# Kernel optimization log

Measured on AMD Instinct MI355X. Metric: run time of the kernel, lower is better.

Reference implementation:

```python
import jax, jax.numpy as jnp
import numpy as np

N1 = 1_000_000
N2 = 1_000_000
C = 64
M = 1_500_000


def setup_inputs() -> dict:
    key = jax.random.key(0)
    k1, k2, k3, k4, k5, k6 = jax.random.split(key, 6)
    feat1 = jax.random.normal(k1, (N1, C), dtype=jnp.float32)
    feat2 = jax.random.normal(k2, (N2, C), dtype=jnp.float32)
    # union_map[0] gathers each input row exactly once -> permutation
    map1_in = jax.random.permutation(k3, N1).astype(jnp.int32)
    map2_in = jax.random.permutation(k4, N2).astype(jnp.int32)
    # union_map[1]: output row each input point lands in
    map1_out = jax.random.randint(k5, (N1,), 0, M, dtype=jnp.int32)
    map2_out = jax.random.randint(k6, (N2,), 0, M, dtype=jnp.int32)
    return {
        "feat1": feat1, "feat2": feat2,
        "map1_in": map1_in, "map1_out": map1_out,
        "map2_in": map2_in, "map2_out": map2_out,
        "out_size": M,
    }


def reference(feat1, feat2, map1_in, map1_out, map2_in, map2_out, out_size):
    # out_feat[union_map[1]] += in_feat[union_map[0]] for each input tensor
    out = jnp.zeros((out_size, feat1.shape[1]), dtype=feat1.dtype)
    out = out.at[map1_out].add(feat1[map1_in])
    out = out.at[map2_out].add(feat2[map2_in])
    return out
```

## Files before the change

kernel.cpp:

```cpp
#include <hip/hip_runtime.h>


#define ROW_C 64
#define TBIT (1 << 30)
#define SCAN_T 256
#define SCAN_PER 16
#define SCAN_CHUNK (SCAN_T * SCAN_PER)

typedef float f32x4 __attribute__((ext_vector_type(4)));
typedef unsigned long long u64;

__device__ __forceinline__ f32x4 feat_load(const float* __restrict__ feat1,
                                           const float* __restrict__ feat2,
                                           int v, int sub) {
    const float* f = (v & TBIT) ? feat2 : feat1;
    int ir = v & (TBIT - 1);
    return *reinterpret_cast<const f32x4*>(f + (size_t)ir * ROW_C + sub);
}

__global__ __launch_bounds__(256) void k_fill_list(
        const int* __restrict__ m1i, const int* __restrict__ m1o,
        const int* __restrict__ m2i, const int* __restrict__ m2o,
        int n1, int n2,
        u64* __restrict__ head, u64* __restrict__ entries) {
    int i = blockIdx.x * blockDim.x + threadIdx.x;
    int r, v;
    if (i < n1) { r = m1o[i]; v = m1i[i]; }
    else {
        int j = i - n1;
        if (j >= n2) return;
        r = m2o[j]; v = m2i[j] | TBIT;
    }
    u64 packed = ((u64)(unsigned)i << 32) | (unsigned)v;
    u64 old = atomicExch(&head[r], packed);
    entries[i] = old;
}

__global__ __launch_bounds__(256) void k_gather_list(
        const float* __restrict__ feat1, const float* __restrict__ feat2,
        const u64* __restrict__ head, const u64* __restrict__ entries,
        float* __restrict__ out, int M) {
    int gid = blockIdx.x * blockDim.x + threadIdx.x;
    int row = gid >> 4;
    if (row >= M) return;
    int sub = (gid & 15) << 2;

    u64 cur = head[row];
    f32x4 acc = {0.f, 0.f, 0.f, 0.f};

    int v0 = (int)(unsigned)cur, v1 = -1, v2 = -1, v3 = -1;
    if (v0 != -1) {
        int nx = (int)(cur >> 32);
        if (nx >= 0) {
            cur = entries[nx]; v1 = (int)(unsigned)cur;
            if (v1 != -1) {
                nx = (int)(cur >> 32);
                if (nx >= 0) {
                    cur = entries[nx]; v2 = (int)(unsigned)cur;
                    if (v2 != -1) {
                        nx = (int)(cur >> 32);
                        if (nx >= 0) {
                            cur = entries[nx]; v3 = (int)(unsigned)cur;
                            if (v3 != -1) {
                                nx = (int)(cur >> 32);
                                while (nx >= 0) {
                                    cur = entries[nx];
                                    int v = (int)(unsigned)cur;
                                    if (v == -1) break;
                                    acc += feat_load(feat1, feat2, v, sub);
                                    nx = (int)(cur >> 32);
                                }
                            }
                        }
                    }
                }
            }
        }
    }

    if (v0 != -1) acc += feat_load(feat1, feat2, v0, sub);
    if (v1 != -1) acc += feat_load(feat1, feat2, v1, sub);
    if (v2 != -1) acc += feat_load(feat1, feat2, v2, sub);
    if (v3 != -1) acc += feat_load(feat1, feat2, v3, sub);

    __builtin_nontemporal_store(acc,
        reinterpret_cast<f32x4*>(out + (size_t)row * ROW_C + sub));
}

__global__ void k_hist(const int* __restrict__ map_out, int n, int* __restrict__ counts) {
    int i = blockIdx.x * blockDim.x + threadIdx.x;
    if (i < n) atomicAdd(&counts[map_out[i]], 1);
}

__global__ void k_partial(const int* __restrict__ counts, int M, int* __restrict__ bsum) {
    __shared__ int lds[SCAN_T];
    int base = blockIdx.x * SCAN_CHUNK + threadIdx.x * SCAN_PER;
    int s = 0;
#pragma unroll
    for (int k = 0; k < SCAN_PER; k++) { int i = base + k; if (i < M) s += counts[i]; }
    lds[threadIdx.x] = s; __syncthreads();
    for (int off = SCAN_T / 2; off > 0; off >>= 1) {
        if (threadIdx.x < off) lds[threadIdx.x] += lds[threadIdx.x + off];
        __syncthreads();
    }
    if (threadIdx.x == 0) bsum[blockIdx.x] = lds[0];
}

__global__ void k_scan_bsum(int* __restrict__ bsum, int nblk) {
    __shared__ int lds[512];
    int t = threadIdx.x;
    lds[t] = (t < nblk) ? bsum[t] : 0;
    __syncthreads();
    for (int off = 1; off < 512; off <<= 1) {
        int v = (t >= off) ? lds[t - off] : 0;
        __syncthreads();
        lds[t] += v;
        __syncthreads();
    }
    if (t < nblk) bsum[t] = (t == 0) ? 0 : lds[t - 1];
}

__global__ void k_offsets(const int* __restrict__ counts, int M,
                          const int* __restrict__ bsum, int* __restrict__ cursor) {
    __shared__ int lds[SCAN_T];
    int base = blockIdx.x * SCAN_CHUNK + threadIdx.x * SCAN_PER;
    int c[SCAN_PER]; int s = 0;
#pragma unroll
    for (int k = 0; k < SCAN_PER; k++) { int i = base + k; c[k] = (i < M) ? counts[i] : 0; s += c[k]; }
    lds[threadIdx.x] = s; __syncthreads();
    for (int off = 1; off < SCAN_T; off <<= 1) {
        int v = (threadIdx.x >= off) ? lds[threadIdx.x - off] : 0;
        __syncthreads();
        lds[threadIdx.x] += v;
        __syncthreads();
    }
    int prefix = bsum[blockIdx.x] + ((threadIdx.x == 0) ? 0 : lds[threadIdx.x - 1]);
#pragma unroll
    for (int k = 0; k < SCAN_PER; k++) { int i = base + k; if (i < M) cursor[i] = prefix; prefix += c[k]; }
}

__global__ void k_fill(const int* __restrict__ map_in, const int* __restrict__ map_out,
                       int n, int tbit, int* __restrict__ cursor, int* __restrict__ csr) {
    int i = blockIdx.x * blockDim.x + threadIdx.x;
    if (i >= n) return;
    int r = map_out[i];
    int pos = atomicAdd(&cursor[r], 1);
    csr[pos] = map_in[i] | tbit;
}

__global__ void k_gather(const float* __restrict__ feat1, const float* __restrict__ feat2,
                         const int* __restrict__ counts, const int* __restrict__ cursor,
                         const int* __restrict__ csr, float* __restrict__ out, int M) {
    int gid = blockIdx.x * blockDim.x + threadIdx.x;
    int row = gid >> 4;
    if (row >= M) return;
    int sub = (gid & 15) << 2;

    int cnt = counts[row];
    int end = cursor[row];
    int start = end - cnt;

    float4 acc = {0.f, 0.f, 0.f, 0.f};
    for (int k = 0; k < cnt; k++) {
        int e = csr[start + k];
        const float* f = (e & TBIT) ? feat2 : feat1;
        int in_r = e & (TBIT - 1);
        float4 v = *reinterpret_cast<const float4*>(f + (size_t)in_r * ROW_C + sub);
        acc.x += v.x; acc.y += v.y; acc.z += v.z; acc.w += v.w;
    }
    *reinterpret_cast<float4*>(out + (size_t)row * ROW_C + sub) = acc;
}

__global__ void scatter_add_rows(const float* __restrict__ feat,
                                 const int* __restrict__ map_in,
                                 const int* __restrict__ map_out,
                                 float* __restrict__ out,
                                 int n_rows) {
    int gid = blockIdx.x * blockDim.x + threadIdx.x;
    int row = gid >> 4;
    if (row >= n_rows) return;
    int sub = (gid & 15) << 2;
    int in_r  = map_in[row];
    int out_r = map_out[row];
    const float4 v = *reinterpret_cast<const float4*>(feat + (size_t)in_r * ROW_C + sub);
    float* o = out + (size_t)out_r * ROW_C + sub;
    unsafeAtomicAdd(o + 0, v.x);
    unsafeAtomicAdd(o + 1, v.y);
    unsafeAtomicAdd(o + 2, v.z);
    unsafeAtomicAdd(o + 3, v.w);
}

extern "C" void kernel_launch(void* const* d_in, const int* in_sizes, int n_in,
                              void* d_out, int out_size, void* d_ws, size_t ws_size,
                              hipStream_t stream) {
    const float* feat1    = (const float*)d_in[0];
    const float* feat2    = (const float*)d_in[1];
    const int*   map1_in  = (const int*)d_in[2];
    const int*   map1_out = (const int*)d_in[3];
    const int*   map2_in  = (const int*)d_in[4];
    const int*   map2_out = (const int*)d_in[5];
    float* out = (float*)d_out;

    const int n1 = in_sizes[2];
    const int n2 = in_sizes[4];
    const int M  = out_size / ROW_C;
    const int ntot = n1 + n2;
    const int block = 256;

    const size_t need_list = ((size_t)M + (size_t)ntot) * sizeof(u64);
    if (ws_size >= need_list) {
        u64* head    = (u64*)d_ws;
        u64* entries = head + M;

        hipMemsetAsync(head, 0xFF, (size_t)M * sizeof(u64), stream);

        int gridf = (ntot + block - 1) / block;
        k_fill_list<<<gridf, block, 0, stream>>>(map1_in, map1_out, map2_in, map2_out,
                                                 n1, n2, head, entries);

        int gridg = (int)(((long long)M * 16 + block - 1) / block);
        k_gather_list<<<gridg, block, 0, stream>>>(feat1, feat2, head, entries, out, M);
        return;
    }

    const int nblk = (M + SCAN_CHUNK - 1) / SCAN_CHUNK;
    const size_t need_csr = (size_t)(2 * (size_t)M + (size_t)ntot + (size_t)nblk) * sizeof(int);
    if (ws_size >= need_csr && nblk <= 512) {
        int* counts = (int*)d_ws;
        int* cursor = counts + M;
        int* csr    = cursor + M;
        int* bsum   = csr + ntot;

        hipMemsetAsync(counts, 0, (size_t)M * sizeof(int), stream);
        k_hist<<<(n1 + block - 1) / block, block, 0, stream>>>(map1_out, n1, counts);
        k_hist<<<(n2 + block - 1) / block, block, 0, stream>>>(map2_out, n2, counts);
        k_partial<<<nblk, SCAN_T, 0, stream>>>(counts, M, bsum);
        k_scan_bsum<<<1, 512, 0, stream>>>(bsum, nblk);
        k_offsets<<<nblk, SCAN_T, 0, stream>>>(counts, M, bsum, cursor);
        k_fill<<<(n1 + block - 1) / block, block, 0, stream>>>(map1_in, map1_out, n1, 0, cursor, csr);
        k_fill<<<(n2 + block - 1) / block, block, 0, stream>>>(map2_in, map2_out, n2, TBIT, cursor, csr);
        int gridg = (int)(((long long)M * 16 + block - 1) / block);
        k_gather<<<gridg, block, 0, stream>>>(feat1, feat2, counts, cursor, csr, out, M);
        return;
    }

    hipMemsetAsync(out, 0, (size_t)out_size * sizeof(float), stream);
    int grid1 = (int)(((long long)n1 * 16 + block - 1) / block);
    int grid2 = (int)(((long long)n2 * 16 + block - 1) / block);
    scatter_add_rows<<<grid1, block, 0, stream>>>(feat1, map1_in, map1_out, out, n1);
    scatter_add_rows<<<grid2, block, 0, stream>>>(feat2, map2_in, map2_out, out, n2);
}
```

Before: 377.8 us.

## Compact linked-list heads into per-row 4-slot records before gather

Adds a compaction kernel that walks each output row's linked list once per row (instead of once per 16 lanes) and writes up to four source indices into an int4 record, with a continuation marker for longer chains. The gather kernel then loads one int4 per row and does independent feature loads without dependent pointer chasing. This trades an extra kernel launch plus a write and read of a 4-int-per-row array for removing the serial dependent entry loads that 16 threads redundantly performed in the gather.

```diff
diff --git a/kernel.cpp b/kernel.cpp
--- a/kernel.cpp
+++ b/kernel.cpp
@@ -3,6 +3,7 @@
 
 #define ROW_C 64
 #define TBIT (1 << 30)
+#define CONT 0x80000000u
 #define SCAN_T 256
 #define SCAN_PER 16
 #define SCAN_CHUNK (SCAN_T * SCAN_PER)
@@ -36,52 +37,70 @@
     entries[i] = old;
 }
 
-__global__ __launch_bounds__(256) void k_gather_list(
+__global__ __launch_bounds__(256) void k_compact(
+        const u64* __restrict__ head, const u64* __restrict__ entries,
+        int* __restrict__ rec, int M) {
+    int r = blockIdx.x * blockDim.x + threadIdx.x;
+    if (r >= M) return;
+    u64 cur = head[r];
+    int s0 = -1, s1 = -1, s2 = -1, s3 = -1;
+    int v = (int)(unsigned)cur;
+    if (v != -1) {
+        s0 = v;
+        cur = entries[(int)(cur >> 32)];
+        v = (int)(unsigned)cur;
+        if (v != -1) {
+            s1 = v;
+            cur = entries[(int)(cur >> 32)];
+            v = (int)(unsigned)cur;
+            if (v != -1) {
+                s2 = v;
+                int nx = (int)(cur >> 32);
+                cur = entries[nx];
+                v = (int)(unsigned)cur;
+                if (v != -1) {
+                    u64 peek = entries[(int)(cur >> 32)];
+                    if ((int)(unsigned)peek == -1) {
+                        s3 = v;
+                    } else {
+                        s3 = (int)(CONT | (unsigned)nx);
+                    }
+                }
+            }
+        }
+    }
+    int4 q = { s0, s1, s2, s3 };
+    *reinterpret_cast<int4*>(rec + ((size_t)r << 2)) = q;
+}
+
+__global__ __launch_bounds__(256) void k_gather_rec4(
         const float* __restrict__ feat1, const float* __restrict__ feat2,
-        const u64* __restrict__ head, const u64* __restrict__ entries,
+        const int* __restrict__ rec, const u64* __restrict__ entries,
         float* __restrict__ out, int M) {
     int gid = blockIdx.x * blockDim.x + threadIdx.x;
     int row = gid >> 4;
     if (row >= M) return;
     int sub = (gid & 15) << 2;
 
-    u64 cur = head[row];
+    const int4 s = *reinterpret_cast<const int4*>(rec + ((size_t)row << 2));
+
     f32x4 acc = {0.f, 0.f, 0.f, 0.f};
-
-    int v0 = (int)(unsigned)cur, v1 = -1, v2 = -1, v3 = -1;
-    if (v0 != -1) {
-        int nx = (int)(cur >> 32);
-        if (nx >= 0) {
-            cur = entries[nx]; v1 = (int)(unsigned)cur;
-            if (v1 != -1) {
-                nx = (int)(cur >> 32);
-                if (nx >= 0) {
-                    cur = entries[nx]; v2 = (int)(unsigned)cur;
-                    if (v2 != -1) {
-                        nx = (int)(cur >> 32);
-                        if (nx >= 0) {
-                            cur = entries[nx]; v3 = (int)(unsigned)cur;
-                            if (v3 != -1) {
-                                nx = (int)(cur >> 32);
-                                while (nx >= 0) {
-                                    cur = entries[nx];
-                                    int v = (int)(unsigned)cur;
-                                    if (v == -1) break;
-                                    acc += feat_load(feat1, feat2, v, sub);
-                                    nx = (int)(cur >> 32);
-                                }
-                            }
-                        }
-                    }
-                }
+    if (s.x != -1) acc += feat_load(feat1, feat2, s.x, sub);
+    if (s.y != -1) acc += feat_load(feat1, feat2, s.y, sub);
+    if (s.z != -1) acc += feat_load(feat1, feat2, s.z, sub);
+    if (s.w != -1) {
+        if ((unsigned)s.w & CONT) {
+            u64 cur = entries[s.w & 0x7FFFFFFF];
+            int v = (int)(unsigned)cur;
+            while (v != -1) {
+                acc += feat_load(feat1, feat2, v, sub);
+                cur = entries[(int)(cur >> 32)];
+                v = (int)(unsigned)cur;
             }
+        } else {
+            acc += feat_load(feat1, feat2, s.w, sub);
         }
     }
-
-    if (v0 != -1) acc += feat_load(feat1, feat2, v0, sub);
-    if (v1 != -1) acc += feat_load(feat1, feat2, v1, sub);
-    if (v2 != -1) acc += feat_load(feat1, feat2, v2, sub);
-    if (v3 != -1) acc += feat_load(feat1, feat2, v3, sub);
 
     __builtin_nontemporal_store(acc,
         reinterpret_cast<f32x4*>(out + (size_t)row * ROW_C + sub));
@@ -207,10 +226,12 @@
     const int ntot = n1 + n2;
     const int block = 256;
 
-    const size_t need_list = ((size_t)M + (size_t)ntot) * sizeof(u64);
+    const size_t need_list = ((size_t)M + (size_t)ntot) * sizeof(u64)
+                           + ((size_t)M * 4) * sizeof(int);
     if (ws_size >= need_list) {
         u64* head    = (u64*)d_ws;
         u64* entries = head + M;
+        int* rec     = (int*)(entries + ntot);
 
         hipMemsetAsync(head, 0xFF, (size_t)M * sizeof(u64), stream);
 
@@ -218,8 +239,11 @@
         k_fill_list<<<gridf, block, 0, stream>>>(map1_in, map1_out, map2_in, map2_out,
                                                  n1, n2, head, entries);
 
+        int gridc = (M + block - 1) / block;
+        k_compact<<<gridc, block, 0, stream>>>(head, entries, rec, M);
+
         int gridg = (int)(((long long)M * 16 + block - 1) / block);
-        k_gather_list<<<gridg, block, 0, stream>>>(feat1, feat2, head, entries, out, M);
+        k_gather_rec4<<<gridg, block, 0, stream>>>(feat1, feat2, rec, entries, out, M);
         return;
     }
 
```

Measured after the change: 327.9 us. 1.15x faster.
